# Kernel tuning notes

Measured on AMD Instinct MI355X. Metric: run time of the kernel, lower is better.

## Reference

```python
import jax, jax.numpy as jnp
import numpy as np

NUM_EXPERT = 8
IN_FEAT = 1024
OUT_FEAT = 1024
N_TOKENS = 8192


def setup_inputs() -> dict:
    key = jax.random.key(0)
    k_inp, k_gate, k_w = jax.random.split(key, 3)
    inp = jax.random.normal(k_inp, (N_TOKENS, IN_FEAT), dtype=jnp.float32)
    gate = jax.random.randint(k_gate, (N_TOKENS,), 0, NUM_EXPERT, dtype=jnp.int32)
    # FMoELinear weight: [num_expert, out_feat, in_feat], kaiming-uniform-like init
    bound = 1.0 / np.sqrt(IN_FEAT)
    weight = jax.random.uniform(
        k_w, (NUM_EXPERT, OUT_FEAT, IN_FEAT), dtype=jnp.float32,
        minval=-bound, maxval=bound)
    return {"inp": inp, "gate": gate, "weight": weight}


def reference(inp, gate, weight):
    # out[i] = weight[gate[i]] @ inp[i]  (top-1 MoE dispatch + grouped GEMM + combine)
    # Loop over the small fixed expert set via scan; each step does a masked
    # dense GEMM so only tokens routed to expert e contribute.
    n, _ = inp.shape
    num_expert, out_feat, _ = weight.shape

    def body(acc, ew):
        e, w_e = ew  # w_e: [out_feat, in_feat]
        mask = (gate == e).astype(inp.dtype)[:, None]  # [n, 1]
        acc = acc + (inp * mask) @ w_e.T               # [n, out_feat]
        return acc, None

    init = jnp.zeros((n, out_feat), dtype=inp.dtype)
    out, _ = jax.lax.scan(body, init, (jnp.arange(num_expert), weight))
    return out
```

## Files before the change

kernel.cpp:

```cpp
#include <hip/hip_runtime.h>
#include <hip/hip_bf16.h>

#define N_TOKENS 8192
#define IN_FEAT 1024
#define OUT_FEAT 1024
#define NUM_EXPERT 8

#define BM 128
#define BN 128
#define BK 32

typedef __bf16 bf16x8 __attribute__((ext_vector_type(8)));
typedef float f32x4 __attribute__((ext_vector_type(4)));

__device__ __forceinline__ unsigned int rne16(float x) {
    union { float f; unsigned int u; } c;
    c.f = x;
    unsigned int u = c.u;
    u += 0x7fffu + ((u >> 16) & 1u);
    return u >> 16;
}
__device__ __forceinline__ unsigned int pk2(float x, float y) {
    return rne16(x) | (rne16(y) << 16);
}

__device__ __forceinline__ bf16x8 cvt8(float4 lo, float4 hi) {
    bf16x8 r;
    r[0] = (__bf16)lo.x; r[1] = (__bf16)lo.y;
    r[2] = (__bf16)lo.z; r[3] = (__bf16)lo.w;
    r[4] = (__bf16)hi.x; r[5] = (__bf16)hi.y;
    r[6] = (__bf16)hi.z; r[7] = (__bf16)hi.w;
    return r;
}

__device__ __forceinline__ void load_lds16(const void* g, void* l) {
    __builtin_amdgcn_global_load_lds(
        (const __attribute__((address_space(1))) unsigned int*)g,
        (__attribute__((address_space(3))) unsigned int*)l,
        16, 0, 0);
}


#define HIST1(G) do { int g_ = (G); unsigned long long m_;                   \
    m_ = __ballot(g_ == 0); c0 += (int)__popcll(m_);                         \
    m_ = __ballot(g_ == 1); c1 += (int)__popcll(m_);                         \
    m_ = __ballot(g_ == 2); c2 += (int)__popcll(m_);                         \
    m_ = __ballot(g_ == 3); c3 += (int)__popcll(m_);                         \
    m_ = __ballot(g_ == 4); c4 += (int)__popcll(m_);                         \
    m_ = __ballot(g_ == 5); c5 += (int)__popcll(m_);                         \
    m_ = __ballot(g_ == 6); c6 += (int)__popcll(m_);                         \
    m_ = __ballot(g_ == 7); c7 += (int)__popcll(m_); } while (0)

#define SCAT1(G, TOK) do { int g_ = (G); int tok_ = (TOK);                   \
    unsigned long long m_;                                                   \
    m_ = __ballot(g_ == 0);                                                  \
    if (g_ == 0) perm[o0 + (int)__popcll(m_ & lt)] = tok_;                   \
    o0 += (int)__popcll(m_);                                                 \
    m_ = __ballot(g_ == 1);                                                  \
    if (g_ == 1) perm[o1 + (int)__popcll(m_ & lt)] = tok_;                   \
    o1 += (int)__popcll(m_);                                                 \
    m_ = __ballot(g_ == 2);                                                  \
    if (g_ == 2) perm[o2 + (int)__popcll(m_ & lt)] = tok_;                   \
    o2 += (int)__popcll(m_);                                                 \
    m_ = __ballot(g_ == 3);                                                  \
    if (g_ == 3) perm[o3 + (int)__popcll(m_ & lt)] = tok_;                   \
    o3 += (int)__popcll(m_);                                                 \
    m_ = __ballot(g_ == 4);                                                  \
    if (g_ == 4) perm[o4 + (int)__popcll(m_ & lt)] = tok_;                   \
    o4 += (int)__popcll(m_);                                                 \
    m_ = __ballot(g_ == 5);                                                  \
    if (g_ == 5) perm[o5 + (int)__popcll(m_ & lt)] = tok_;                   \
    o5 += (int)__popcll(m_);                                                 \
    m_ = __ballot(g_ == 6);                                                  \
    if (g_ == 6) perm[o6 + (int)__popcll(m_ & lt)] = tok_;                   \
    o6 += (int)__popcll(m_);                                                 \
    m_ = __ballot(g_ == 7);                                                  \
    if (g_ == 7) perm[o7 + (int)__popcll(m_ & lt)] = tok_;                   \
    o7 += (int)__popcll(m_); } while (0)

__device__ __forceinline__ void sort_core(const int* __restrict__ gate,
                                          int* __restrict__ perm,
                                          int* __restrict__ seg,
                                          int* whist, int* wbase) {
    const int t = threadIdx.x;
    const int wave = t >> 6, lane = t & 63;
    const unsigned long long lt = (lane == 0) ? 0ull : (~0ull >> (64 - lane));

    int c0 = 0, c1 = 0, c2 = 0, c3 = 0, c4 = 0, c5 = 0, c6 = 0, c7 = 0;
    #pragma unroll
    for (int j = 0; j < 8; ++j) {
        int4 vv = ((const int4*)gate)[j * 256 + t];
        HIST1(vv.x); HIST1(vv.y); HIST1(vv.z); HIST1(vv.w);
    }
    if (lane == 0) {
        whist[wave * 8 + 0] = c0; whist[wave * 8 + 1] = c1;
        whist[wave * 8 + 2] = c2; whist[wave * 8 + 3] = c3;
        whist[wave * 8 + 4] = c4; whist[wave * 8 + 5] = c5;
        whist[wave * 8 + 6] = c6; whist[wave * 8 + 7] = c7;
    }
    __syncthreads();

    if (t == 0) {
        int s = 0;
        #pragma unroll
        for (int e = 0; e < NUM_EXPERT; ++e) {
            seg[e] = s;
            int b = s;
            #pragma unroll
            for (int w = 0; w < 4; ++w) { wbase[w * 8 + e] = b; b += whist[w * 8 + e]; }
            s = b;
        }
        seg[NUM_EXPERT] = s;
    }
    __syncthreads();

    int o0 = wbase[wave * 8 + 0], o1 = wbase[wave * 8 + 1];
    int o2 = wbase[wave * 8 + 2], o3 = wbase[wave * 8 + 3];
    int o4 = wbase[wave * 8 + 4], o5 = wbase[wave * 8 + 5];
    int o6 = wbase[wave * 8 + 6], o7 = wbase[wave * 8 + 7];
    #pragma unroll
    for (int j = 0; j < 8; ++j) {
        int4 vv = ((const int4*)gate)[j * 256 + t];
        const int tb = j * 1024 + t * 4;
        SCAT1(vv.x, tb);
        SCAT1(vv.y, tb + 1);
        SCAT1(vv.z, tb + 2);
        SCAT1(vv.w, tb + 3);
    }
}

__global__ __launch_bounds__(256) void moe_sort(const int* __restrict__ gate,
                                                int* __restrict__ perm,
                                                int* __restrict__ seg) {
    __shared__ int whist[4 * NUM_EXPERT];
    __shared__ int wbase[4 * NUM_EXPERT];
    sort_core(gate, perm, seg, whist, wbase);
}

__global__ __launch_bounds__(256) void moe_prep_sort(
    const float* __restrict__ inp,
    const float* __restrict__ weight,
    const int* __restrict__ gate,
    int* __restrict__ perm,
    int* __restrict__ seg,
    unsigned int* __restrict__ A2,
    unsigned int* __restrict__ W2) {

    const int bid = blockIdx.x;
    if (bid == 0) {
        __shared__ int whist[4 * NUM_EXPERT];
        __shared__ int wbase[4 * NUM_EXPERT];
        sort_core(gate, perm, seg, whist, wbase);
        return;
    }
    const int cid = bid - 1;
    const int t = threadIdx.x;
    const int wave = t >> 6, lane = t & 63;
    const float* src;
    unsigned int* dst;
    if (cid < 2048) {
        int row = cid * 4 + wave;
        src = inp + row * IN_FEAT;
        dst = A2 + row * (IN_FEAT / 2);
    } else {
        int row = (cid - 2048) * 4 + wave;
        src = weight + row * IN_FEAT;
        dst = W2 + row * (IN_FEAT / 2);
    }
    #pragma unroll
    for (int j = 0; j < 4; ++j) {
        float4 v = *(const float4*)(src + j * 256 + lane * 4);
        uint2 o;
        o.x = pk2(v.x, v.y);
        o.y = pk2(v.z, v.w);
        *(uint2*)(dst + j * 128 + lane * 2) = o;
    }
}

__global__ __launch_bounds__(256, 2) void moe_gemm(
    const unsigned short* __restrict__ A2,
    const unsigned short* __restrict__ W2,
    const int* __restrict__ perm,
    const int* __restrict__ seg,
    float* __restrict__ out) {

    const int bid = blockIdx.x;
    const int e = bid & 7;
    const int ntile = (bid >> 3) & 7;
    const int mtile = bid >> 6;

    const int base = seg[e];
    const int cnt = seg[e + 1] - base;
    if (mtile * BM >= cnt) return;
    const int tbase = base + mtile * BM;
    int rows = cnt - mtile * BM; if (rows > BM) rows = BM;

    __shared__ __align__(16) unsigned short lA[2][2][BM * BK];
    __shared__ __align__(16) unsigned short lB[2][2][BN * BK];

    const int t = threadIdx.x;

    const int crow = t >> 2;
    const int p = (t & 3) ^ (crow & 3);
    int ar0 = tbase + crow;       if (ar0 > N_TOKENS - 1) ar0 = N_TOKENS - 1;
    int ar1 = tbase + 64 + crow;  if (ar1 > N_TOKENS - 1) ar1 = N_TOKENS - 1;
    const unsigned short* gA0 = A2 + (size_t)perm[ar0] * IN_FEAT + p * 8;
    const unsigned short* gA1 = A2 + (size_t)perm[ar1] * IN_FEAT + p * 8;
    const unsigned short* gB0 = W2 + (size_t)e * (OUT_FEAT * IN_FEAT)
                                + (ntile * BN + crow) * IN_FEAT + p * 8;
    const unsigned short* gB1 = gB0 + 64 * IN_FEAT;
    const int dofs = t * 8;
    const int dofs2 = (t + 256) * 8;

    const int wave = t >> 6;
    const int lane = t & 63;
    const int wm = (wave & 1) << 6;
    const int wn = (wave >> 1) << 6;
    const int l15 = lane & 15;
    const int quad = lane >> 4;
    const int qx = quad ^ (l15 & 3);
    const int fofsA = (wm + l15) * BK + qx * 8;
    const int fofsB = (wn + l15) * BK + qx * 8;

    f32x4 acc[4][4];
    #pragma unroll
    for (int i = 0; i < 4; ++i)
        #pragma unroll
        for (int j = 0; j < 4; ++j)
            acc[i][j] = (f32x4)0.0f;

    #define STAGE(s, buf, half) do {                                         \
        load_lds16(gA0 + (s) * 32, &lA[buf][half][dofs]);                    \
        load_lds16(gA1 + (s) * 32, &lA[buf][half][dofs2]);                   \
        load_lds16(gB0 + (s) * 32, &lB[buf][half][dofs]);                    \
        load_lds16(gB1 + (s) * 32, &lB[buf][half][dofs2]);                   \
    } while (0)

    #define COMPUTE(buf, half) do {                                          \
        bf16x8 af[4], bq[4];                                                 \
        _Pragma("unroll")                                                    \
        for (int i = 0; i < 4; ++i)                                          \
            af[i] = *(const bf16x8*)&lA[buf][half][fofsA + i * 16 * BK];     \
        _Pragma("unroll")                                                    \
        for (int j = 0; j < 4; ++j)                                          \
            bq[j] = *(const bf16x8*)&lB[buf][half][fofsB + j * 16 * BK];     \
        _Pragma("unroll")                                                    \
        for (int i = 0; i < 4; ++i)                                          \
            _Pragma("unroll")                                                \
            for (int j = 0; j < 4; ++j)                                      \
                acc[i][j] = __builtin_amdgcn_mfma_f32_16x16x32_bf16(         \
                    af[i], bq[j], acc[i][j], 0, 0, 0);                       \
    } while (0)

    STAGE(0, 0, 0);
    STAGE(1, 0, 1);

    #pragma unroll 1
    for (int i = 0; i < 16; ++i) {
        const int b = i & 1;
        __syncthreads();
        if (i < 15) {
            if (b == 0) { STAGE(2 * i + 2, 1, 0); STAGE(2 * i + 3, 1, 1); }
            else        { STAGE(2 * i + 2, 0, 0); STAGE(2 * i + 3, 0, 1); }
        }
        if (b == 0) { COMPUTE(0, 0); COMPUTE(0, 1); }
        else        { COMPUTE(1, 0); COMPUTE(1, 1); }
    }

    #undef STAGE
    #undef COMPUTE

    #pragma unroll
    for (int mi = 0; mi < 4; ++mi) {
        #pragma unroll
        for (int r = 0; r < 4; ++r) {
            int row = wm + mi * 16 + quad * 4 + r;
            if (row < rows) {
                int token = perm[tbase + row];
                float* op = out + token * OUT_FEAT + ntile * BN + wn;
                #pragma unroll
                for (int ni = 0; ni < 4; ++ni)
                    op[ni * 16 + l15] = acc[mi][ni][r];
            }
        }
    }
}

__global__ __launch_bounds__(256, 2) void moe_gemm_f(
    const float* __restrict__ inp,
    const float* __restrict__ weight,
    const int* __restrict__ perm,
    const int* __restrict__ seg,
    float* __restrict__ out) {

    const int bid = blockIdx.x;
    const int e = bid & 7;
    const int ntile = (bid >> 3) & 7;
    const int mtile = bid >> 6;

    const int base = seg[e];
    const int cnt = seg[e + 1] - base;
    if (mtile * BM >= cnt) return;
    const int tbase = base + mtile * BM;
    int rows = cnt - mtile * BM; if (rows > BM) rows = BM;

    __shared__ __align__(16) unsigned short lA[2][BM * BK];
    __shared__ __align__(16) unsigned short lB[2][BN * BK];

    const int t = threadIdx.x;
    const int crow = t >> 2;
    const int p = (t & 3) ^ (crow & 3);
    int ar0 = tbase + crow;       if (ar0 > N_TOKENS - 1) ar0 = N_TOKENS - 1;
    int ar1 = tbase + 64 + crow;  if (ar1 > N_TOKENS - 1) ar1 = N_TOKENS - 1;
    const float* gA0 = inp + (size_t)perm[ar0] * IN_FEAT + p * 8;
    const float* gA1 = inp + (size_t)perm[ar1] * IN_FEAT + p * 8;
    const float* gB0 = weight + (size_t)e * (OUT_FEAT * IN_FEAT)
                       + (ntile * BN + crow) * IN_FEAT + p * 8;
    const float* gB1 = gB0 + 64 * IN_FEAT;
    const int dofs = t * 8;
    const int dofs2 = (t + 256) * 8;

    const int wave = t >> 6;
    const int lane = t & 63;
    const int wm = (wave & 1) << 6;
    const int wn = (wave >> 1) << 6;
    const int l15 = lane & 15;
    const int quad = lane >> 4;
    const int qx = quad ^ (l15 & 3);
    const int fofsA = (wm + l15) * BK + qx * 8;
    const int fofsB = (wn + l15) * BK + qx * 8;

    f32x4 acc[4][4];
    #pragma unroll
    for (int i = 0; i < 4; ++i)
        #pragma unroll
        for (int j = 0; j < 4; ++j)
            acc[i][j] = (f32x4)0.0f;

    float4 ra0, ra1, ra2, ra3, rb0, rb1, rb2, rb3;

    ra0 = *(const float4*)(gA0);     ra1 = *(const float4*)(gA0 + 4);
    ra2 = *(const float4*)(gA1);     ra3 = *(const float4*)(gA1 + 4);
    rb0 = *(const float4*)(gB0);     rb1 = *(const float4*)(gB0 + 4);
    rb2 = *(const float4*)(gB1);     rb3 = *(const float4*)(gB1 + 4);
    *(bf16x8*)&lA[0][dofs]  = cvt8(ra0, ra1);
    *(bf16x8*)&lA[0][dofs2] = cvt8(ra2, ra3);
    *(bf16x8*)&lB[0][dofs]  = cvt8(rb0, rb1);
    *(bf16x8*)&lB[0][dofs2] = cvt8(rb2, rb3);

    #pragma unroll 1
    for (int s = 0; s < 32; ++s) {
        const int cur = s & 1;
        const int k0 = (s + 1) * BK;

        if (s < 31) {
            ra0 = *(const float4*)(gA0 + k0);     ra1 = *(const float4*)(gA0 + k0 + 4);
            ra2 = *(const float4*)(gA1 + k0);     ra3 = *(const float4*)(gA1 + k0 + 4);
            rb0 = *(const float4*)(gB0 + k0);     rb1 = *(const float4*)(gB0 + k0 + 4);
            rb2 = *(const float4*)(gB1 + k0);     rb3 = *(const float4*)(gB1 + k0 + 4);
        }

        __syncthreads();

        {
            bf16x8 af[4], bq[4];
            #pragma unroll
            for (int i = 0; i < 4; ++i)
                af[i] = *(const bf16x8*)&lA[cur][fofsA + i * 16 * BK];
            #pragma unroll
            for (int j = 0; j < 4; ++j)
                bq[j] = *(const bf16x8*)&lB[cur][fofsB + j * 16 * BK];
            #pragma unroll
            for (int i = 0; i < 4; ++i)
                #pragma unroll
                for (int j = 0; j < 4; ++j)
                    acc[i][j] = __builtin_amdgcn_mfma_f32_16x16x32_bf16(
                        af[i], bq[j], acc[i][j], 0, 0, 0);
        }

        if (s < 31) {
            *(bf16x8*)&lA[cur ^ 1][dofs]  = cvt8(ra0, ra1);
            *(bf16x8*)&lA[cur ^ 1][dofs2] = cvt8(ra2, ra3);
            *(bf16x8*)&lB[cur ^ 1][dofs]  = cvt8(rb0, rb1);
            *(bf16x8*)&lB[cur ^ 1][dofs2] = cvt8(rb2, rb3);
        }
    }

    #pragma unroll
    for (int mi = 0; mi < 4; ++mi) {
        #pragma unroll
        for (int r = 0; r < 4; ++r) {
            int row = wm + mi * 16 + quad * 4 + r;
            if (row < rows) {
                int token = perm[tbase + row];
                float* op = out + token * OUT_FEAT + ntile * BN + wn;
                #pragma unroll
                for (int ni = 0; ni < 4; ++ni)
                    op[ni * 16 + l15] = acc[mi][ni][r];
            }
        }
    }
}

extern "C" void kernel_launch(void* const* d_in, const int* in_sizes, int n_in,
                              void* d_out, int out_size, void* d_ws, size_t ws_size,
                              hipStream_t stream) {
    const float* inp = (const float*)d_in[0];
    const int* gate = (const int*)d_in[1];
    const float* weight = (const float*)d_in[2];
    float* out = (float*)d_out;

    int* perm = (int*)d_ws;
    int* seg = perm + N_TOKENS;

    const size_t need = 65536 + 2ull * N_TOKENS * IN_FEAT * 2;
    if (ws_size >= need) {
        unsigned int* A2 = (unsigned int*)((char*)d_ws + 65536);
        unsigned int* W2 = A2 + (N_TOKENS * IN_FEAT / 2);
        moe_prep_sort<<<4097, 256, 0, stream>>>(inp, weight, gate, perm, seg,
                                                A2, W2);
        moe_gemm<<<4096, 256, 0, stream>>>((const unsigned short*)A2,
                                           (const unsigned short*)W2,
                                           perm, seg, out);
    } else {
        moe_sort<<<1, 256, 0, stream>>>(gate, perm, seg);
        moe_gemm_f<<<4096, 256, 0, stream>>>(inp, weight, perm, seg, out);
    }
}
```

Before: 152.0 us.

## Switch GEMM mainloop to 3-stage ring buffer with partial vmcnt waits

```diff
diff --git a/kernel.cpp b/kernel.cpp
--- a/kernel.cpp
+++ b/kernel.cpp
@@ -39,7 +39,6 @@
         (__attribute__((address_space(3))) unsigned int*)l,
         16, 0, 0);
 }
-
 
 #define HIST1(G) do { int g_ = (G); unsigned long long m_;                   \
     m_ = __ballot(g_ == 0); c0 += (int)__popcll(m_);                         \
@@ -177,7 +176,7 @@
     }
 }
 
-__global__ __launch_bounds__(256, 2) void moe_gemm(
+__global__ __launch_bounds__(256, 3) void moe_gemm(
     const unsigned short* __restrict__ A2,
     const unsigned short* __restrict__ W2,
     const int* __restrict__ perm,
@@ -195,13 +194,13 @@
     const int tbase = base + mtile * BM;
     int rows = cnt - mtile * BM; if (rows > BM) rows = BM;
 
-    __shared__ __align__(16) unsigned short lA[2][2][BM * BK];
-    __shared__ __align__(16) unsigned short lB[2][2][BN * BK];
+    __shared__ __align__(16) unsigned short lA[3][BM * BK];
+    __shared__ __align__(16) unsigned short lB[3][BN * BK];
 
     const int t = threadIdx.x;
 
     const int crow = t >> 2;
-    const int p = (t & 3) ^ (crow & 3);
+    const int p = (t & 3) ^ (crow & 3) ^ ((crow >> 2) & 3);
     int ar0 = tbase + crow;       if (ar0 > N_TOKENS - 1) ar0 = N_TOKENS - 1;
     int ar1 = tbase + 64 + crow;  if (ar1 > N_TOKENS - 1) ar1 = N_TOKENS - 1;
     const unsigned short* gA0 = A2 + (size_t)perm[ar0] * IN_FEAT + p * 8;
@@ -218,7 +217,7 @@
     const int wn = (wave >> 1) << 6;
     const int l15 = lane & 15;
     const int quad = lane >> 4;
-    const int qx = quad ^ (l15 & 3);
+    const int qx = quad ^ (l15 & 3) ^ ((l15 >> 2) & 3);
     const int fofsA = (wm + l15) * BK + qx * 8;
     const int fofsB = (wn + l15) * BK + qx * 8;
 
@@ -229,21 +228,21 @@
         for (int j = 0; j < 4; ++j)
             acc[i][j] = (f32x4)0.0f;
 
-    #define STAGE(s, buf, half) do {                                         \
-        load_lds16(gA0 + (s) * 32, &lA[buf][half][dofs]);                    \
-        load_lds16(gA1 + (s) * 32, &lA[buf][half][dofs2]);                   \
-        load_lds16(gB0 + (s) * 32, &lB[buf][half][dofs]);                    \
-        load_lds16(gB1 + (s) * 32, &lB[buf][half][dofs2]);                   \
+    #define STAGE(s, b) do {                                                 \
+        load_lds16(gA0 + (s) * 32, &lA[b][dofs]);                            \
+        load_lds16(gA1 + (s) * 32, &lA[b][dofs2]);                           \
+        load_lds16(gB0 + (s) * 32, &lB[b][dofs]);                            \
+        load_lds16(gB1 + (s) * 32, &lB[b][dofs2]);                           \
     } while (0)
 
-    #define COMPUTE(buf, half) do {                                          \
+    #define COMPUTE(b) do {                                                  \
         bf16x8 af[4], bq[4];                                                 \
         _Pragma("unroll")                                                    \
         for (int i = 0; i < 4; ++i)                                          \
-            af[i] = *(const bf16x8*)&lA[buf][half][fofsA + i * 16 * BK];     \
+            af[i] = *(const bf16x8*)&lA[b][fofsA + i * 16 * BK];             \
         _Pragma("unroll")                                                    \
         for (int j = 0; j < 4; ++j)                                          \
-            bq[j] = *(const bf16x8*)&lB[buf][half][fofsB + j * 16 * BK];     \
+            bq[j] = *(const bf16x8*)&lB[b][fofsB + j * 16 * BK];             \
         _Pragma("unroll")                                                    \
         for (int i = 0; i < 4; ++i)                                          \
             _Pragma("unroll")                                                \
@@ -252,20 +251,25 @@
                     af[i], bq[j], acc[i][j], 0, 0, 0);                       \
     } while (0)
 
-    STAGE(0, 0, 0);
-    STAGE(1, 0, 1);
-
+    STAGE(0, 0);
+    STAGE(1, 1);
+
+    int cur = 0;
+    int stg = 2;
     #pragma unroll 1
-    for (int i = 0; i < 16; ++i) {
-        const int b = i & 1;
-        __syncthreads();
-        if (i < 15) {
-            if (b == 0) { STAGE(2 * i + 2, 1, 0); STAGE(2 * i + 3, 1, 1); }
-            else        { STAGE(2 * i + 2, 0, 0); STAGE(2 * i + 3, 0, 1); }
-        }
-        if (b == 0) { COMPUTE(0, 0); COMPUTE(0, 1); }
-        else        { COMPUTE(1, 0); COMPUTE(1, 1); }
-    }
+    for (int s = 0; s < 30; ++s) {
+        asm volatile("s_waitcnt vmcnt(4)" ::: "memory");
+        __builtin_amdgcn_s_barrier();
+        __builtin_amdgcn_sched_barrier(0);
+        STAGE(s + 2, stg);
+        COMPUTE(cur);
+        cur = (cur == 2) ? 0 : cur + 1;
+        stg = (stg == 2) ? 0 : stg + 1;
+    }
+    __syncthreads();
+    COMPUTE(0);
+    __syncthreads();
+    COMPUTE(1);
 
     #undef STAGE
     #undef COMPUTE
```

Measured after the change: 142.6 us, median of 2. -6.2%, faster.

## Fuse activation bf16 conversion into GEMM by loading fp32 A into registers

Applied to the files above, without the earlier changes.

```diff
diff --git a/kernel.cpp b/kernel.cpp
--- a/kernel.cpp
+++ b/kernel.cpp
@@ -39,7 +39,6 @@
         (__attribute__((address_space(3))) unsigned int*)l,
         16, 0, 0);
 }
-
 
 #define HIST1(G) do { int g_ = (G); unsigned long long m_;                   \
     m_ = __ballot(g_ == 0); c0 += (int)__popcll(m_);                         \
@@ -138,12 +137,10 @@
 }
 
 __global__ __launch_bounds__(256) void moe_prep_sort(
-    const float* __restrict__ inp,
     const float* __restrict__ weight,
     const int* __restrict__ gate,
     int* __restrict__ perm,
     int* __restrict__ seg,
-    unsigned int* __restrict__ A2,
     unsigned int* __restrict__ W2) {
 
     const int bid = blockIdx.x;
@@ -156,17 +153,9 @@
     const int cid = bid - 1;
     const int t = threadIdx.x;
     const int wave = t >> 6, lane = t & 63;
-    const float* src;
-    unsigned int* dst;
-    if (cid < 2048) {
-        int row = cid * 4 + wave;
-        src = inp + row * IN_FEAT;
-        dst = A2 + row * (IN_FEAT / 2);
-    } else {
-        int row = (cid - 2048) * 4 + wave;
-        src = weight + row * IN_FEAT;
-        dst = W2 + row * (IN_FEAT / 2);
-    }
+    const int row = cid * 4 + wave;
+    const float* src = weight + (size_t)row * IN_FEAT;
+    unsigned int* dst = W2 + (size_t)row * (IN_FEAT / 2);
     #pragma unroll
     for (int j = 0; j < 4; ++j) {
         float4 v = *(const float4*)(src + j * 256 + lane * 4);
@@ -178,7 +167,7 @@
 }
 
 __global__ __launch_bounds__(256, 2) void moe_gemm(
-    const unsigned short* __restrict__ A2,
+    const float* __restrict__ inp,
     const unsigned short* __restrict__ W2,
     const int* __restrict__ perm,
     const int* __restrict__ seg,
@@ -195,17 +184,12 @@
     const int tbase = base + mtile * BM;
     int rows = cnt - mtile * BM; if (rows > BM) rows = BM;
 
-    __shared__ __align__(16) unsigned short lA[2][2][BM * BK];
-    __shared__ __align__(16) unsigned short lB[2][2][BN * BK];
+    __shared__ __align__(16) unsigned short lB[2][BN * BK];
 
     const int t = threadIdx.x;
 
     const int crow = t >> 2;
-    const int p = (t & 3) ^ (crow & 3);
-    int ar0 = tbase + crow;       if (ar0 > N_TOKENS - 1) ar0 = N_TOKENS - 1;
-    int ar1 = tbase + 64 + crow;  if (ar1 > N_TOKENS - 1) ar1 = N_TOKENS - 1;
-    const unsigned short* gA0 = A2 + (size_t)perm[ar0] * IN_FEAT + p * 8;
-    const unsigned short* gA1 = A2 + (size_t)perm[ar1] * IN_FEAT + p * 8;
+    const int p = (t & 3) ^ (crow & 3) ^ ((crow >> 2) & 3);
     const unsigned short* gB0 = W2 + (size_t)e * (OUT_FEAT * IN_FEAT)
                                 + (ntile * BN + crow) * IN_FEAT + p * 8;
     const unsigned short* gB1 = gB0 + 64 * IN_FEAT;
@@ -218,9 +202,17 @@
     const int wn = (wave >> 1) << 6;
     const int l15 = lane & 15;
     const int quad = lane >> 4;
-    const int qx = quad ^ (l15 & 3);
-    const int fofsA = (wm + l15) * BK + qx * 8;
+    const int qx = quad ^ (l15 & 3) ^ ((l15 >> 2) & 3);
     const int fofsB = (wn + l15) * BK + qx * 8;
+
+    int r0 = tbase + wm + l15;        if (r0 > N_TOKENS - 1) r0 = N_TOKENS - 1;
+    int r1 = r0 + 16;                 if (r1 > N_TOKENS - 1) r1 = N_TOKENS - 1;
+    int r2 = r0 + 32;                 if (r2 > N_TOKENS - 1) r2 = N_TOKENS - 1;
+    int r3 = r0 + 48;                 if (r3 > N_TOKENS - 1) r3 = N_TOKENS - 1;
+    const float* a0p = inp + (size_t)perm[r0] * IN_FEAT + quad * 8;
+    const float* a1p = inp + (size_t)perm[r1] * IN_FEAT + quad * 8;
+    const float* a2p = inp + (size_t)perm[r2] * IN_FEAT + quad * 8;
+    const float* a3p = inp + (size_t)perm[r3] * IN_FEAT + quad * 8;
 
     f32x4 acc[4][4];
     #pragma unroll
@@ -229,46 +221,58 @@
         for (int j = 0; j < 4; ++j)
             acc[i][j] = (f32x4)0.0f;
 
-    #define STAGE(s, buf, half) do {                                         \
-        load_lds16(gA0 + (s) * 32, &lA[buf][half][dofs]);                    \
-        load_lds16(gA1 + (s) * 32, &lA[buf][half][dofs2]);                   \
-        load_lds16(gB0 + (s) * 32, &lB[buf][half][dofs]);                    \
-        load_lds16(gB1 + (s) * 32, &lB[buf][half][dofs2]);                   \
+    #define STAGEW(s, b) do {                                                \
+        load_lds16(gB0 + (s) * 32, &lB[b][dofs]);                            \
+        load_lds16(gB1 + (s) * 32, &lB[b][dofs2]);                           \
     } while (0)
 
-    #define COMPUTE(buf, half) do {                                          \
-        bf16x8 af[4], bq[4];                                                 \
-        _Pragma("unroll")                                                    \
-        for (int i = 0; i < 4; ++i)                                          \
-            af[i] = *(const bf16x8*)&lA[buf][half][fofsA + i * 16 * BK];     \
-        _Pragma("unroll")                                                    \
-        for (int j = 0; j < 4; ++j)                                          \
-            bq[j] = *(const bf16x8*)&lB[buf][half][fofsB + j * 16 * BK];     \
-        _Pragma("unroll")                                                    \
-        for (int i = 0; i < 4; ++i)                                          \
-            _Pragma("unroll")                                                \
-            for (int j = 0; j < 4; ++j)                                      \
-                acc[i][j] = __builtin_amdgcn_mfma_f32_16x16x32_bf16(         \
-                    af[i], bq[j], acc[i][j], 0, 0, 0);                       \
+    #define LOADA(s) do { const int ko = (s) * 32;                           \
+        al0 = *(const float4*)(a0p + ko); ah0 = *(const float4*)(a0p + ko + 4); \
+        al1 = *(const float4*)(a1p + ko); ah1 = *(const float4*)(a1p + ko + 4); \
+        al2 = *(const float4*)(a2p + ko); ah2 = *(const float4*)(a2p + ko + 4); \
+        al3 = *(const float4*)(a3p + ko); ah3 = *(const float4*)(a3p + ko + 4); \
     } while (0)
 
-    STAGE(0, 0, 0);
-    STAGE(1, 0, 1);
+    float4 al0, ah0, al1, ah1, al2, ah2, al3, ah3;
+
+    STAGEW(0, 0);
+    LOADA(0);
 
     #pragma unroll 1
-    for (int i = 0; i < 16; ++i) {
-        const int b = i & 1;
+    for (int s = 0; s < 32; ++s) {
+        const int cur = s & 1;
+
         __syncthreads();
-        if (i < 15) {
-            if (b == 0) { STAGE(2 * i + 2, 1, 0); STAGE(2 * i + 3, 1, 1); }
-            else        { STAGE(2 * i + 2, 0, 0); STAGE(2 * i + 3, 0, 1); }
-        }
-        if (b == 0) { COMPUTE(0, 0); COMPUTE(0, 1); }
-        else        { COMPUTE(1, 0); COMPUTE(1, 1); }
-    }
-
-    #undef STAGE
-    #undef COMPUTE
+
+        if (s < 31) STAGEW(s + 1, cur ^ 1);
+
+        bf16x8 af0 = cvt8(al0, ah0);
+        bf16x8 af1 = cvt8(al1, ah1);
+        bf16x8 af2 = cvt8(al2, ah2);
+        bf16x8 af3 = cvt8(al3, ah3);
+        if (s < 31) LOADA(s + 1);
+
+        {
+            bf16x8 bq[4];
+            #pragma unroll
+            for (int j = 0; j < 4; ++j)
+                bq[j] = *(const bf16x8*)&lB[cur][fofsB + j * 16 * BK];
+            #pragma unroll
+            for (int j = 0; j < 4; ++j) {
+                acc[0][j] = __builtin_amdgcn_mfma_f32_16x16x32_bf16(
+                    af0, bq[j], acc[0][j], 0, 0, 0);
+                acc[1][j] = __builtin_amdgcn_mfma_f32_16x16x32_bf16(
+                    af1, bq[j], acc[1][j], 0, 0, 0);
+                acc[2][j] = __builtin_amdgcn_mfma_f32_16x16x32_bf16(
+                    af2, bq[j], acc[2][j], 0, 0, 0);
+                acc[3][j] = __builtin_amdgcn_mfma_f32_16x16x32_bf16(
+                    af3, bq[j], acc[3][j], 0, 0, 0);
+            }
+        }
+    }
+
+    #undef STAGEW
+    #undef LOADA
 
     #pragma unroll
     for (int mi = 0; mi < 4; ++mi) {
@@ -413,14 +417,11 @@
     int* perm = (int*)d_ws;
     int* seg = perm + N_TOKENS;
 
-    const size_t need = 65536 + 2ull * N_TOKENS * IN_FEAT * 2;
+    const size_t need = 65536 + (size_t)NUM_EXPERT * OUT_FEAT * IN_FEAT * 2;
     if (ws_size >= need) {
-        unsigned int* A2 = (unsigned int*)((char*)d_ws + 65536);
-        unsigned int* W2 = A2 + (N_TOKENS * IN_FEAT / 2);
-        moe_prep_sort<<<4097, 256, 0, stream>>>(inp, weight, gate, perm, seg,
-                                                A2, W2);
-        moe_gemm<<<4096, 256, 0, stream>>>((const unsigned short*)A2,
-                                           (const unsigned short*)W2,
+        unsigned int* W2 = (unsigned int*)((char*)d_ws + 65536);
+        moe_prep_sort<<<2049, 256, 0, stream>>>(weight, gate, perm, seg, W2);
+        moe_gemm<<<4096, 256, 0, stream>>>(inp, (const unsigned short*)W2,
                                            perm, seg, out);
     } else {
         moe_sort<<<1, 256, 0, stream>>>(gate, perm, seg);
```

After: 216.2 us. 1.42x slower.
